# Kernel optimization log

Measured on AMD Instinct MI355X. Metric: run time of the kernel, lower is better.

## Reference

```python
import jax, jax.numpy as jnp
import numpy as np

B, T, D_IN, H, D2, D_OUT, N_CULT = 1024, 128, 32, 512, 256, 16, 32


def setup_inputs() -> dict:
    key = jax.random.key(0)
    ks = jax.random.split(key, 16)
    s = 0.05
    return {
        "input": jax.random.normal(ks[0], (B, T, D_IN), jnp.float32),
        "hn": jnp.zeros((1, B, H), jnp.float32),
        "cultivars": jax.random.randint(ks[1], (B, 1), 0, N_CULT, jnp.int32),
        "W1": jax.random.normal(ks[2], (D2, D_IN), jnp.float32) * s,
        "b1": jnp.zeros((D2,), jnp.float32),
        "W2": jax.random.normal(ks[3], (H, D2), jnp.float32) * s,
        "b2": jnp.zeros((H,), jnp.float32),
        "W_ih": jax.random.normal(ks[4], (3 * H, H), jnp.float32) * s,
        "W_hh": jax.random.normal(ks[5], (3 * H, H), jnp.float32) * s,
        "b_ih": jnp.zeros((3 * H,), jnp.float32),
        "b_hh": jnp.zeros((3 * H,), jnp.float32),
        "W3": jax.random.normal(ks[6], (D2, H), jnp.float32) * s,
        "b3": jnp.zeros((D2,), jnp.float32),
        "Wh": jax.random.normal(ks[7], (N_CULT, D_OUT, D2), jnp.float32) * s,
        "bh": jnp.zeros((N_CULT, D_OUT), jnp.float32),
    }


def _gru(x, h0, W_ih, W_hh, b_ih, b_hh):
    # x: [B,T,H]; h0: [B,H]. PyTorch GRU gate order: r, z, n.
    gx = jnp.einsum('bth,gh->btg', x, W_ih) + b_ih  # [B,T,3H]
    gx = jnp.swapaxes(gx, 0, 1)  # [T,B,3H]

    def step(h, gx_t):
        gh = h @ W_hh.T + b_hh
        xr, xz, xn = jnp.split(gx_t, 3, axis=-1)
        hr, hz, hnn = jnp.split(gh, 3, axis=-1)
        r = jax.nn.sigmoid(xr + hr)
        z = jax.nn.sigmoid(xz + hz)
        n = jnp.tanh(xn + r * hnn)
        h_new = (1.0 - z) * n + z * h
        return h_new, None

    h_last, _ = jax.lax.scan(step, h0, gx)
    return h_last  # [B,H]


def reference(input, hn, cultivars, W1, b1, W2, b2, W_ih, W_hh, b_ih, b_hh, W3, b3, Wh, bh):
    x = input @ W1.T + b1          # [B,T,D2]
    x = x @ W2.T + b2              # [B,T,H]
    h_last = _gru(x, hn[0], W_ih, W_hh, b_ih, b_hh)  # [B,H]
    hn_out = h_last[None]          # [1,B,H]
    out = jax.nn.relu(hn_out)
    out = jax.nn.relu(out @ W3.T + b3)[0]  # [B,D2]
    cult = cultivars[:, 0]
    # grouped per-sample head: params[i] = Wh[cult[i]] @ out[i] + bh[cult[i]]
    params = jnp.einsum('bd,bod->bo', out, Wh[cult]) + bh[cult]  # [B,D_OUT]
    return (params, hn_out)
```

## Files before the change

### kernel.cpp

```cpp
#include <hip/hip_runtime.h>


#define T_STEPS 128
#define PITCH   516
#define SLAB_ROWS 32

typedef __attribute__((ext_vector_type(8))) short short8;
typedef __attribute__((ext_vector_type(4))) float f32x4;
typedef __attribute__((ext_vector_type(4))) float float4v;
typedef unsigned short u16;
typedef unsigned long long u64;

static __device__ __forceinline__ u16 f2bf(float f) {
    unsigned int u = __builtin_bit_cast(unsigned int, f);
    u += 0x7FFFu + ((u >> 16) & 1u);
    return (u16)(u >> 16);
}
static __device__ __forceinline__ f32x4 mfma16(short8 a, short8 b, f32x4 c) {
    return __builtin_amdgcn_mfma_f32_16x16x32_bf16(a, b, c, 0, 0, 0);
}
static __device__ __forceinline__ void st_h16(u16* p, short8 v) {
    struct W { u64 a, b; } w = __builtin_bit_cast(W, v);
    u64* q = (u64*)p;
    __hip_atomic_store(q + 0, w.a, __ATOMIC_RELAXED, __HIP_MEMORY_SCOPE_AGENT);
    __hip_atomic_store(q + 1, w.b, __ATOMIC_RELAXED, __HIP_MEMORY_SCOPE_AGENT);
}
static __device__ __forceinline__ u64 ld_sc1_u64(const u16* p) {
    return __hip_atomic_load((const u64*)p, __ATOMIC_RELAXED, __HIP_MEMORY_SCOPE_AGENT);
}
static __device__ __forceinline__ short8 lds8(const u16* p) {
    u64 lo = *(const u64*)p;
    u64 hi = *(const u64*)(p + 4);
    struct W { u64 a, b; } w{lo, hi};
    return __builtin_bit_cast(short8, w);
}

#define WS_HBUF0 0
#define WS_HBUF1 1048576
#define WS_W21   2097152
#define WS_B21   2162688
#define WS_WEFF  2164736
#define WS_BEFF  2263040
#define WS_FLAGS 2269184

__global__ void k_prep0(const float* __restrict__ W1, const float* __restrict__ b1,
                        const float* __restrict__ W2, const float* __restrict__ b2,
                        float* __restrict__ W21, float* __restrict__ b21,
                        unsigned* __restrict__ flags) {
    if (blockIdx.x == 0)
        __hip_atomic_store(&flags[threadIdx.x], 0u, __ATOMIC_RELAXED, __HIP_MEMORY_SCOPE_AGENT);
    int gid = blockIdx.x * 256 + threadIdx.x;
    int k = gid >> 5, d = gid & 31;
    float acc = 0.f;
    for (int j = 0; j < 256; ++j)
        acc += W2[k * 256 + j] * W1[j * 32 + d];
    W21[k * 32 + d] = acc;
    if (d == 0) {
        float bb = b2[k];
        for (int j = 0; j < 256; ++j) bb += W2[k * 256 + j] * b1[j];
        b21[k] = bb;
    }
}

__global__ void k_prep1(const float* __restrict__ W_ih, const float* __restrict__ b_ih,
                        const float* __restrict__ W21, const float* __restrict__ b21,
                        u16* __restrict__ Weff, float* __restrict__ beff) {
    int gid = blockIdx.x * 256 + threadIdx.x;
    int g = gid >> 5, d = gid & 31;
    float acc = 0.f;
    for (int k = 0; k < 512; ++k)
        acc += W_ih[g * 512 + k] * W21[k * 32 + d];
    Weff[g * 32 + d] = f2bf(acc);
    if (d == 0) {
        float bb = b_ih[g];
        for (int k = 0; k < 512; ++k) bb += W_ih[g * 512 + k] * b21[k];
        beff[g] = bb;
    }
}

static __device__ __forceinline__ void bar_arrive(unsigned* gflags, int slot, unsigned v) {
    __syncthreads();
    if (threadIdx.x == 0)
        __hip_atomic_store(&gflags[slot], v, __ATOMIC_RELAXED, __HIP_MEMORY_SCOPE_AGENT);
}
static __device__ __forceinline__ void bar_wait(const unsigned* gflags, unsigned v) {
    if (threadIdx.x < 64) {
        int idx = threadIdx.x & 7;
        for (;;) {
            unsigned f = __hip_atomic_load(&gflags[idx], __ATOMIC_RELAXED, __HIP_MEMORY_SCOPE_AGENT);
            if (__ballot(f >= v) == ~0ull) break;
            __builtin_amdgcn_s_sleep(1);
        }
    }
    __syncthreads();
}

__launch_bounds__(256, 1)
__global__ void k_gru(const float* __restrict__ input, const float* __restrict__ hn,
                      const float* __restrict__ W_hh, const float* __restrict__ b_hh,
                      const u16* __restrict__ Weff, const float* __restrict__ beff,
                      u16* __restrict__ hbuf0, u16* __restrict__ hbuf1,
                      unsigned* __restrict__ flags, float* __restrict__ hn_out) {
    __shared__ __align__(16) u16 slab[SLAB_ROWS * PITCH];

    const int tid  = threadIdx.x;
    const int wave = tid >> 6, lane = tid & 63;
    const int col_l = lane & 15, quad = lane >> 4;
    const int blk = blockIdx.x;
    const int grp = blk & 31, colg = blk >> 5;
    const int grpbase = grp * 32;
    const int cb = colg * 64 + wave * 16;
    unsigned* gflags = flags + grp * 8;

    {
        int b = grpbase + colg * 4 + wave;
        const float* src = hn + (size_t)b * 512 + lane * 8;
        short8 v;
        #pragma unroll
        for (int e = 0; e < 8; ++e) v[e] = (short)f2bf(src[e]);
        st_h16(hbuf0 + (size_t)b * 512 + lane * 8, v);
    }
    short8 whhf[3][16];
    #pragma unroll
    for (int g3 = 0; g3 < 3; ++g3) {
        const float* wrow = W_hh + (size_t)(g3 * 512 + cb + col_l) * 512;
        #pragma unroll
        for (int kc = 0; kc < 16; ++kc) {
            const float* p = wrow + kc * 32 + quad * 8;
            short8 v;
            #pragma unroll
            for (int e = 0; e < 8; ++e) v[e] = (short)f2bf(p[e]);
            whhf[g3][kc] = v;
        }
    }
    short8 bwx[3];
    float bx[3], bhh[3];
    #pragma unroll
    for (int g3 = 0; g3 < 3; ++g3) {
        int nr = g3 * 512 + cb + col_l;
        bwx[g3] = *(const short8*)(Weff + nr * 32 + quad * 8);
        bx[g3]  = beff[nr];
        bhh[g3] = b_hh[nr];
    }
    float hs[2][4];
    #pragma unroll
    for (int m = 0; m < 2; ++m)
        #pragma unroll
        for (int i = 0; i < 4; ++i)
            hs[m][i] = hn[(size_t)(grpbase + m * 16 + quad * 4 + i) * 512 + cb + col_l];

    bar_arrive(gflags, colg, 1u);

    u16* bufs[2] = { hbuf0, hbuf1 };
    #pragma unroll 1
    for (int t = 0; t < T_STEPS; ++t) {
        const u16* hsrc = bufs[t & 1];
        u16* hdst = bufs[(t + 1) & 1];

        float xf[2][8];
        #pragma unroll
        for (int m = 0; m < 2; ++m) {
            const float* xp = input + (size_t)(grpbase + m * 16 + col_l) * 4096 + t * 32 + quad * 8;
            float4v a = *(const float4v*)xp;
            float4v b = *(const float4v*)(xp + 4);
            #pragma unroll
            for (int e = 0; e < 4; ++e) { xf[m][e] = a[e]; xf[m][4 + e] = b[e]; }
        }

        bar_wait(gflags, (unsigned)(t + 1));

        {
            u64 stg[16];
            #pragma unroll
            for (int r8 = 0; r8 < 8; ++r8) {
                int r = (wave * 8 + r8 + colg * 4) & 31;
                #pragma unroll
                for (int j = 0; j < 2; ++j)
                    stg[r8 * 2 + j] = ld_sc1_u64(hsrc + (size_t)(grpbase + r) * 512 + j * 256 + lane * 4);
            }
            #pragma unroll
            for (int r8 = 0; r8 < 8; ++r8) {
                int r = (wave * 8 + r8 + colg * 4) & 31;
                #pragma unroll
                for (int j = 0; j < 2; ++j)
                    *(u64*)&slab[r * PITCH + j * 256 + lane * 4] = stg[r8 * 2 + j];
            }
        }
        __syncthreads();

        #pragma unroll
        for (int m = 0; m < 2; ++m) {
            short8 ax;
            #pragma unroll
            for (int e = 0; e < 8; ++e) ax[e] = (short)f2bf(xf[m][e]);
            f32x4 z4 = { 0.f, 0.f, 0.f, 0.f };
            f32x4 ar  = mfma16(ax, bwx[0], z4);
            f32x4 az  = mfma16(ax, bwx[1], z4);
            f32x4 anx = mfma16(ax, bwx[2], z4);
            f32x4 anh = z4;
            const int arow = (m * 16 + col_l) * PITCH;
            #pragma unroll
            for (int kc = 0; kc < 16; ++kc) {
                short8 a = lds8(slab + arow + kc * 32 + quad * 8);
                ar  = mfma16(a, whhf[0][kc], ar);
                az  = mfma16(a, whhf[1][kc], az);
                anh = mfma16(a, whhf[2][kc], anh);
            }
            #pragma unroll
            for (int i = 0; i < 4; ++i) {
                float r = 1.f / (1.f + __expf(-(ar[i] + bx[0] + bhh[0])));
                float z = 1.f / (1.f + __expf(-(az[i] + bx[1] + bhh[1])));
                float np = anx[i] + bx[2] + r * (anh[i] + bhh[2]);
                float e  = __expf(-2.f * fabsf(np));
                float nn = __builtin_copysignf((1.f - e) / (1.f + e), np);
                float h  = (1.f - z) * nn + z * hs[m][i];
                hs[m][i] = h;
                int b = grpbase + m * 16 + quad * 4 + i;
                __hip_atomic_store(&hdst[(size_t)b * 512 + cb + col_l], f2bf(h),
                                   __ATOMIC_RELAXED, __HIP_MEMORY_SCOPE_AGENT);
            }
        }
        if (t < T_STEPS - 1)
            bar_arrive(gflags, colg, (unsigned)(t + 2));
    }
    #pragma unroll
    for (int m = 0; m < 2; ++m)
        #pragma unroll
        for (int i = 0; i < 4; ++i)
            hn_out[(size_t)(grpbase + m * 16 + quad * 4 + i) * 512 + cb + col_l] = hs[m][i];
}

__launch_bounds__(256)
__global__ void k_head(const u16* __restrict__ hfin, const float* __restrict__ W3,
                       const float* __restrict__ b3, const int* __restrict__ cult,
                       const float* __restrict__ Wh, const float* __restrict__ bh,
                       float* __restrict__ params) {
    __shared__ float out2[16][264];
    const int tid = threadIdx.x, wave = tid >> 6, lane = tid & 63;
    const int col_l = lane & 15, quad = lane >> 4;
    const int bbase = blockIdx.x * 16;

    f32x4 z4 = { 0.f, 0.f, 0.f, 0.f };
    f32x4 acc[4];
    #pragma unroll
    for (int nt = 0; nt < 4; ++nt) acc[nt] = z4;

    #pragma unroll
    for (int kc = 0; kc < 16; ++kc) {
        short8 a = *(const short8*)(hfin + (size_t)(bbase + col_l) * 512 + kc * 32 + quad * 8);
        #pragma unroll
        for (int e = 0; e < 8; ++e) {
            u16 v = (u16)a[e];
            a[e] = (short)((v & 0x8000u) ? 0 : v);
        }
        #pragma unroll
        for (int nt = 0; nt < 4; ++nt) {
            int nrow = wave * 64 + nt * 16 + col_l;
            const float* wr = W3 + (size_t)nrow * 512 + kc * 32 + quad * 8;
            short8 b;
            #pragma unroll
            for (int e = 0; e < 8; ++e) b[e] = (short)f2bf(wr[e]);
            acc[nt] = mfma16(a, b, acc[nt]);
        }
    }
    #pragma unroll
    for (int nt = 0; nt < 4; ++nt) {
        int ncol = wave * 64 + nt * 16 + col_l;
        float bias = b3[ncol];
        #pragma unroll
        for (int i = 0; i < 4; ++i) {
            float v = acc[nt][i] + bias;
            out2[quad * 4 + i][ncol] = v > 0.f ? v : 0.f;
        }
    }
    __syncthreads();
    int b_local = tid >> 4, o2 = tid & 15;
    int batch = bbase + b_local;
    int c = cult[batch];
    float acc2 = bh[c * 16 + o2];
    const float* wrow = Wh + (size_t)(c * 16 + o2) * 256;
    for (int d = 0; d < 256; ++d) acc2 += out2[b_local][d] * wrow[d];
    params[(size_t)batch * 16 + o2] = acc2;
}

extern "C" void kernel_launch(void* const* d_in, const int* in_sizes, int n_in,
                              void* d_out, int out_size, void* d_ws, size_t ws_size,
                              hipStream_t stream) {
    (void)in_sizes; (void)n_in; (void)out_size; (void)ws_size;
    const float* input = (const float*)d_in[0];
    const float* hn    = (const float*)d_in[1];
    const int*   cult  = (const int*)d_in[2];
    const float* W1    = (const float*)d_in[3];
    const float* b1    = (const float*)d_in[4];
    const float* W2    = (const float*)d_in[5];
    const float* b2    = (const float*)d_in[6];
    const float* W_ih  = (const float*)d_in[7];
    const float* W_hh  = (const float*)d_in[8];
    const float* b_ih  = (const float*)d_in[9];
    const float* b_hh  = (const float*)d_in[10];
    const float* W3    = (const float*)d_in[11];
    const float* b3    = (const float*)d_in[12];
    const float* Wh    = (const float*)d_in[13];
    const float* bh    = (const float*)d_in[14];

    char* ws = (char*)d_ws;
    u16*      hbuf0 = (u16*)(ws + WS_HBUF0);
    u16*      hbuf1 = (u16*)(ws + WS_HBUF1);
    float*    W21   = (float*)(ws + WS_W21);
    float*    b21   = (float*)(ws + WS_B21);
    u16*      Weff  = (u16*)(ws + WS_WEFF);
    float*    beff  = (float*)(ws + WS_BEFF);
    unsigned* flags = (unsigned*)(ws + WS_FLAGS);

    float* out    = (float*)d_out;
    float* params = out;
    float* hnout  = out + 16384;

    k_prep0<<<64, 256, 0, stream>>>(W1, b1, W2, b2, W21, b21, flags);
    k_prep1<<<192, 256, 0, stream>>>(W_ih, b_ih, W21, b21, Weff, beff);
    k_gru<<<256, 256, 0, stream>>>(input, hn, W_hh, b_hh, Weff, beff,
                                   hbuf0, hbuf1, flags, hnout);
    k_head<<<64, 256, 0, stream>>>(hbuf0, W3, b3, cult, Wh, bh, params);
}
```

Baseline: 741.8 us.

## Split GRU batch groups into 16-row groups across 512 blocks

Doubles the number of persistent GRU blocks from 256 to 512 by halving the batch rows each block handles (16 instead of 32), with 64 groups of 8 column blocks. Launch bounds are raised to allow two blocks per CU, and the input-projection MFMAs are hoisted before the barrier wait so they overlap the spin. Each block now reloads its W_hh slice into registers while doing half the recurrent work per step, which shortens the serial per-step path. The costs are more barrier flags, doubled total W_hh register loading, and co-residency requirements for the spin barrier under the higher register pressure of two blocks per CU.

```diff
diff --git a/kernel.cpp b/kernel.cpp
--- a/kernel.cpp
+++ b/kernel.cpp
@@ -3,7 +3,7 @@
 
 #define T_STEPS 128
 #define PITCH   516
-#define SLAB_ROWS 32
+#define SLAB_ROWS 16
 
 typedef __attribute__((ext_vector_type(8))) short short8;
 typedef __attribute__((ext_vector_type(4))) float f32x4;
@@ -47,8 +47,10 @@
                         const float* __restrict__ W2, const float* __restrict__ b2,
                         float* __restrict__ W21, float* __restrict__ b21,
                         unsigned* __restrict__ flags) {
-    if (blockIdx.x == 0)
+    if (blockIdx.x == 0) {
         __hip_atomic_store(&flags[threadIdx.x], 0u, __ATOMIC_RELAXED, __HIP_MEMORY_SCOPE_AGENT);
+        __hip_atomic_store(&flags[256 + threadIdx.x], 0u, __ATOMIC_RELAXED, __HIP_MEMORY_SCOPE_AGENT);
+    }
     int gid = blockIdx.x * 256 + threadIdx.x;
     int k = gid >> 5, d = gid & 31;
     float acc = 0.f;
@@ -95,7 +97,7 @@
     __syncthreads();
 }
 
-__launch_bounds__(256, 1)
+__launch_bounds__(256, 2)
 __global__ void k_gru(const float* __restrict__ input, const float* __restrict__ hn,
                       const float* __restrict__ W_hh, const float* __restrict__ b_hh,
                       const u16* __restrict__ Weff, const float* __restrict__ beff,
@@ -107,18 +109,22 @@
     const int wave = tid >> 6, lane = tid & 63;
     const int col_l = lane & 15, quad = lane >> 4;
     const int blk = blockIdx.x;
-    const int grp = blk & 31, colg = blk >> 5;
-    const int grpbase = grp * 32;
+    const int grp = (blk & 31) | ((blk >> 8) << 5);
+    const int colg = (blk >> 5) & 7;
+    const int grpbase = grp * 16;
     const int cb = colg * 64 + wave * 16;
     unsigned* gflags = flags + grp * 8;
 
-    {
-        int b = grpbase + colg * 4 + wave;
-        const float* src = hn + (size_t)b * 512 + lane * 8;
-        short8 v;
-        #pragma unroll
-        for (int e = 0; e < 8; ++e) v[e] = (short)f2bf(src[e]);
-        st_h16(hbuf0 + (size_t)b * 512 + lane * 8, v);
+    if (colg == 0) {
+        #pragma unroll
+        for (int r4 = 0; r4 < 4; ++r4) {
+            int b = grpbase + wave * 4 + r4;
+            const float* src = hn + (size_t)b * 512 + lane * 8;
+            short8 v;
+            #pragma unroll
+            for (int e = 0; e < 8; ++e) v[e] = (short)f2bf(src[e]);
+            st_h16(hbuf0 + (size_t)b * 512 + lane * 8, v);
+        }
     }
     short8 whhf[3][16];
     #pragma unroll
@@ -142,12 +148,10 @@
         bx[g3]  = beff[nr];
         bhh[g3] = b_hh[nr];
     }
-    float hs[2][4];
-    #pragma unroll
-    for (int m = 0; m < 2; ++m)
-        #pragma unroll
-        for (int i = 0; i < 4; ++i)
-            hs[m][i] = hn[(size_t)(grpbase + m * 16 + quad * 4 + i) * 512 + cb + col_l];
+    float hs[4];
+    #pragma unroll
+    for (int i = 0; i < 4; ++i)
+        hs[i] = hn[(size_t)(grpbase + quad * 4 + i) * 512 + cb + col_l];
 
     bar_arrive(gflags, colg, 1u);
 
@@ -157,77 +161,68 @@
         const u16* hsrc = bufs[t & 1];
         u16* hdst = bufs[(t + 1) & 1];
 
-        float xf[2][8];
-        #pragma unroll
-        for (int m = 0; m < 2; ++m) {
-            const float* xp = input + (size_t)(grpbase + m * 16 + col_l) * 4096 + t * 32 + quad * 8;
+        short8 ax;
+        {
+            const float* xp = input + (size_t)(grpbase + col_l) * 4096 + t * 32 + quad * 8;
             float4v a = *(const float4v*)xp;
             float4v b = *(const float4v*)(xp + 4);
             #pragma unroll
-            for (int e = 0; e < 4; ++e) { xf[m][e] = a[e]; xf[m][4 + e] = b[e]; }
-        }
+            for (int e = 0; e < 4; ++e) { ax[e] = (short)f2bf(a[e]); ax[4 + e] = (short)f2bf(b[e]); }
+        }
+        f32x4 z4 = { 0.f, 0.f, 0.f, 0.f };
+        f32x4 ar  = mfma16(ax, bwx[0], z4);
+        f32x4 az  = mfma16(ax, bwx[1], z4);
+        f32x4 anx = mfma16(ax, bwx[2], z4);
+        f32x4 anh = z4;
 
         bar_wait(gflags, (unsigned)(t + 1));
 
         {
-            u64 stg[16];
-            #pragma unroll
-            for (int r8 = 0; r8 < 8; ++r8) {
-                int r = (wave * 8 + r8 + colg * 4) & 31;
+            u64 stg[8];
+            #pragma unroll
+            for (int r4 = 0; r4 < 4; ++r4) {
+                int r = (wave * 4 + r4 + colg * 2) & 15;
                 #pragma unroll
                 for (int j = 0; j < 2; ++j)
-                    stg[r8 * 2 + j] = ld_sc1_u64(hsrc + (size_t)(grpbase + r) * 512 + j * 256 + lane * 4);
+                    stg[r4 * 2 + j] = ld_sc1_u64(hsrc + (size_t)(grpbase + r) * 512 + j * 256 + lane * 4);
             }
             #pragma unroll
-            for (int r8 = 0; r8 < 8; ++r8) {
-                int r = (wave * 8 + r8 + colg * 4) & 31;
+            for (int r4 = 0; r4 < 4; ++r4) {
+                int r = (wave * 4 + r4 + colg * 2) & 15;
                 #pragma unroll
                 for (int j = 0; j < 2; ++j)
-                    *(u64*)&slab[r * PITCH + j * 256 + lane * 4] = stg[r8 * 2 + j];
+                    *(u64*)&slab[r * PITCH + j * 256 + lane * 4] = stg[r4 * 2 + j];
             }
         }
         __syncthreads();
 
-        #pragma unroll
-        for (int m = 0; m < 2; ++m) {
-            short8 ax;
-            #pragma unroll
-            for (int e = 0; e < 8; ++e) ax[e] = (short)f2bf(xf[m][e]);
-            f32x4 z4 = { 0.f, 0.f, 0.f, 0.f };
-            f32x4 ar  = mfma16(ax, bwx[0], z4);
-            f32x4 az  = mfma16(ax, bwx[1], z4);
-            f32x4 anx = mfma16(ax, bwx[2], z4);
-            f32x4 anh = z4;
-            const int arow = (m * 16 + col_l) * PITCH;
-            #pragma unroll
-            for (int kc = 0; kc < 16; ++kc) {
-                short8 a = lds8(slab + arow + kc * 32 + quad * 8);
-                ar  = mfma16(a, whhf[0][kc], ar);
-                az  = mfma16(a, whhf[1][kc], az);
-                anh = mfma16(a, whhf[2][kc], anh);
-            }
-            #pragma unroll
-            for (int i = 0; i < 4; ++i) {
-                float r = 1.f / (1.f + __expf(-(ar[i] + bx[0] + bhh[0])));
-                float z = 1.f / (1.f + __expf(-(az[i] + bx[1] + bhh[1])));
-                float np = anx[i] + bx[2] + r * (anh[i] + bhh[2]);
-                float e  = __expf(-2.f * fabsf(np));
-                float nn = __builtin_copysignf((1.f - e) / (1.f + e), np);
-                float h  = (1.f - z) * nn + z * hs[m][i];
-                hs[m][i] = h;
-                int b = grpbase + m * 16 + quad * 4 + i;
-                __hip_atomic_store(&hdst[(size_t)b * 512 + cb + col_l], f2bf(h),
-                                   __ATOMIC_RELAXED, __HIP_MEMORY_SCOPE_AGENT);
-            }
+        const int arow = col_l * PITCH;
+        #pragma unroll
+        for (int kc = 0; kc < 16; ++kc) {
+            short8 a = lds8(slab + arow + kc * 32 + quad * 8);
+            ar  = mfma16(a, whhf[0][kc], ar);
+            az  = mfma16(a, whhf[1][kc], az);
+            anh = mfma16(a, whhf[2][kc], anh);
+        }
+        #pragma unroll
+        for (int i = 0; i < 4; ++i) {
+            float r = 1.f / (1.f + __expf(-(ar[i] + bx[0] + bhh[0])));
+            float z = 1.f / (1.f + __expf(-(az[i] + bx[1] + bhh[1])));
+            float np = anx[i] + bx[2] + r * (anh[i] + bhh[2]);
+            float e  = __expf(-2.f * fabsf(np));
+            float nn = __builtin_copysignf((1.f - e) / (1.f + e), np);
+            float h  = (1.f - z) * nn + z * hs[i];
+            hs[i] = h;
+            int b = grpbase + quad * 4 + i;
+            __hip_atomic_store(&hdst[(size_t)b * 512 + cb + col_l], f2bf(h),
+                               __ATOMIC_RELAXED, __HIP_MEMORY_SCOPE_AGENT);
         }
         if (t < T_STEPS - 1)
             bar_arrive(gflags, colg, (unsigned)(t + 2));
     }
     #pragma unroll
-    for (int m = 0; m < 2; ++m)
-        #pragma unroll
-        for (int i = 0; i < 4; ++i)
-            hn_out[(size_t)(grpbase + m * 16 + quad * 4 + i) * 512 + cb + col_l] = hs[m][i];
+    for (int i = 0; i < 4; ++i)
+        hn_out[(size_t)(grpbase + quad * 4 + i) * 512 + cb + col_l] = hs[i];
 }
 
 __launch_bounds__(256)
@@ -318,7 +313,7 @@
 
     k_prep0<<<64, 256, 0, stream>>>(W1, b1, W2, b2, W21, b21, flags);
     k_prep1<<<192, 256, 0, stream>>>(W_ih, b_ih, W21, b21, Weff, beff);
-    k_gru<<<256, 256, 0, stream>>>(input, hn, W_hh, b_hh, Weff, beff,
+    k_gru<<<512, 256, 0, stream>>>(input, hn, W_hh, b_hh, Weff, beff,
                                    hbuf0, hbuf1, flags, hnout);
     k_head<<<64, 256, 0, stream>>>(hbuf0, W3, b3, cult, Wh, bh, params);
 }
```

Result: slower. 779.9 us (+5.1%).

## Add runtime-probed fast per-step barrier using workgroup-scope atomics and direct LDS DMA

Applied to the files above, without the earlier changes.

At startup each group of 8 blocks checks whether plain (non-coherent) global writes from its partner blocks become visible, using a token write and read-back through global-to-LDS DMA. If the check passes, the per-step sync switches to workgroup-scope atomics and plain stores, and the hidden-state slab is pulled straight into LDS with global_load_lds instead of going through registers. The input-projection MFMAs are also issued before the barrier wait so they overlap it, and the LDS pitch changes for 16-byte reads. The risk is correctness: it bets that the 8 blocks of a group share a cache. The visibility probe may pass by chance while later steps read stale data.

```diff
diff --git a/kernel.cpp b/kernel.cpp
--- a/kernel.cpp
+++ b/kernel.cpp
@@ -2,7 +2,7 @@
 
 
 #define T_STEPS 128
-#define PITCH   516
+#define PITCH   520
 #define SLAB_ROWS 32
 
 typedef __attribute__((ext_vector_type(8))) short short8;
@@ -11,6 +11,13 @@
 typedef unsigned short u16;
 typedef unsigned long long u64;
 
+#define DMA16(g, l) __builtin_amdgcn_global_load_lds( \
+    (const __attribute__((address_space(1))) void*)(g), \
+    (__attribute__((address_space(3))) void*)(l), 16, 0, 1)
+#define DMA4(g, l) __builtin_amdgcn_global_load_lds( \
+    (const __attribute__((address_space(1))) void*)(g), \
+    (__attribute__((address_space(3))) void*)(l), 4, 0, 1)
+
 static __device__ __forceinline__ u16 f2bf(float f) {
     unsigned int u = __builtin_bit_cast(unsigned int, f);
     u += 0x7FFFu + ((u >> 16) & 1u);
@@ -27,12 +34,6 @@
 }
 static __device__ __forceinline__ u64 ld_sc1_u64(const u16* p) {
     return __hip_atomic_load((const u64*)p, __ATOMIC_RELAXED, __HIP_MEMORY_SCOPE_AGENT);
-}
-static __device__ __forceinline__ short8 lds8(const u16* p) {
-    u64 lo = *(const u64*)p;
-    u64 hi = *(const u64*)(p + 4);
-    struct W { u64 a, b; } w{lo, hi};
-    return __builtin_bit_cast(short8, w);
 }
 
 #define WS_HBUF0 0
@@ -41,14 +42,21 @@
 #define WS_B21   2162688
 #define WS_WEFF  2164736
 #define WS_BEFF  2263040
-#define WS_FLAGS 2269184
+#define WS_SFLAG 2269184
+#define WS_FFLAG 2270208
+#define WS_TEST  2274304
+#define WS_OK    2282496
+#define WS_TOKS  2283520
 
 __global__ void k_prep0(const float* __restrict__ W1, const float* __restrict__ b1,
                         const float* __restrict__ W2, const float* __restrict__ b2,
                         float* __restrict__ W21, float* __restrict__ b21,
-                        unsigned* __restrict__ flags) {
-    if (blockIdx.x == 0)
-        __hip_atomic_store(&flags[threadIdx.x], 0u, __ATOMIC_RELAXED, __HIP_MEMORY_SCOPE_AGENT);
+                        unsigned* __restrict__ sflags, unsigned* __restrict__ fflags) {
+    if (blockIdx.x == 0) {
+        int t = threadIdx.x;
+        __hip_atomic_store(&sflags[t], 0u, __ATOMIC_RELAXED, __HIP_MEMORY_SCOPE_AGENT);
+        __hip_atomic_store(&fflags[(t >> 3) * 32 + (t & 7)], 0u, __ATOMIC_RELAXED, __HIP_MEMORY_SCOPE_AGENT);
+    }
     int gid = blockIdx.x * 256 + threadIdx.x;
     int k = gid >> 5, d = gid & 31;
     float acc = 0.f;
@@ -78,12 +86,12 @@
     }
 }
 
-static __device__ __forceinline__ void bar_arrive(unsigned* gflags, int slot, unsigned v) {
+static __device__ __forceinline__ void bar_arrive_slow(unsigned* gflags, int slot, unsigned v) {
     __syncthreads();
     if (threadIdx.x == 0)
         __hip_atomic_store(&gflags[slot], v, __ATOMIC_RELAXED, __HIP_MEMORY_SCOPE_AGENT);
 }
-static __device__ __forceinline__ void bar_wait(const unsigned* gflags, unsigned v) {
+static __device__ __forceinline__ void bar_wait_slow(const unsigned* gflags, unsigned v) {
     if (threadIdx.x < 64) {
         int idx = threadIdx.x & 7;
         for (;;) {
@@ -94,14 +102,30 @@
     }
     __syncthreads();
 }
+static __device__ __forceinline__ void bar_wait_fast(unsigned* gff, unsigned v) {
+    if (threadIdx.x < 64) {
+        for (;;) {
+            unsigned f = v;
+            if (threadIdx.x < 8)
+                f = __hip_atomic_fetch_add(&gff[threadIdx.x], 0u,
+                                           __ATOMIC_RELAXED, __HIP_MEMORY_SCOPE_WORKGROUP);
+            if (__ballot(f >= v) == ~0ull) break;
+            __builtin_amdgcn_s_sleep(1);
+        }
+    }
+    __syncthreads();
+}
 
 __launch_bounds__(256, 1)
 __global__ void k_gru(const float* __restrict__ input, const float* __restrict__ hn,
                       const float* __restrict__ W_hh, const float* __restrict__ b_hh,
                       const u16* __restrict__ Weff, const float* __restrict__ beff,
                       u16* __restrict__ hbuf0, u16* __restrict__ hbuf1,
-                      unsigned* __restrict__ flags, float* __restrict__ hn_out) {
+                      unsigned* __restrict__ sflags, unsigned* __restrict__ fflags,
+                      unsigned* __restrict__ testc, unsigned* __restrict__ okbuf,
+                      unsigned* __restrict__ tokslot, float* __restrict__ hn_out) {
     __shared__ __align__(16) u16 slab[SLAB_ROWS * PITCH];
+    __shared__ unsigned fast_sh;
 
     const int tid  = threadIdx.x;
     const int wave = tid >> 6, lane = tid & 63;
@@ -110,7 +134,9 @@
     const int grp = blk & 31, colg = blk >> 5;
     const int grpbase = grp * 32;
     const int cb = colg * 64 + wave * 16;
-    unsigned* gflags = flags + grp * 8;
+    unsigned* gflags = sflags + grp * 8;
+    unsigned* gff    = fflags + grp * 32;
+    unsigned* trow   = testc + grp * 64;
 
     {
         int b = grpbase + colg * 4 + wave;
@@ -120,6 +146,16 @@
         for (int e = 0; e < 8; ++e) v[e] = (short)f2bf(src[e]);
         st_h16(hbuf0 + (size_t)b * 512 + lane * 8, v);
     }
+    unsigned tok = 0;
+    if (colg == 0) {
+        u64 rt = __builtin_amdgcn_s_memrealtime();
+        tok = ((unsigned)rt ^ (unsigned)(rt >> 32)) | 1u;
+        if (tid < 64) trow[tid] = tok;
+        if (tid == 0)
+            __hip_atomic_store(&tokslot[grp], tok, __ATOMIC_RELAXED, __HIP_MEMORY_SCOPE_AGENT);
+    }
+    bar_arrive_slow(gflags, colg, 1u);
+
     short8 whhf[3][16];
     #pragma unroll
     for (int g3 = 0; g3 < 3; ++g3) {
@@ -149,7 +185,34 @@
         for (int i = 0; i < 4; ++i)
             hs[m][i] = hn[(size_t)(grpbase + m * 16 + quad * 4 + i) * 512 + cb + col_l];
 
-    bar_arrive(gflags, colg, 1u);
+    bar_wait_slow(gflags, 1u);
+    unsigned tokv = __hip_atomic_load(&tokslot[grp], __ATOMIC_RELAXED, __HIP_MEMORY_SCOPE_AGENT);
+    unsigned* hsk = (unsigned*)slab;
+    if (tid < 64) DMA4(trow + lane, hsk + lane);
+    bar_arrive_slow(gflags, colg, 2u);
+    bar_wait_slow(gflags, 2u);
+    if (colg == 0 && tid < 64) trow[tid] = tokv + 1u;
+    bar_arrive_slow(gflags, colg, 3u);
+    bar_wait_slow(gflags, 3u);
+    if (tid < 64) DMA4(trow + lane, hsk + 64 + lane);
+    __syncthreads();
+    if (tid < 64) {
+        unsigned ok = (hsk[64 + lane] == tokv + 1u) ? 1u : 0u;
+        unsigned allok = (__ballot(ok != 0u) == ~0ull) ? 1u : 0u;
+        if (tid == 0)
+            __hip_atomic_store(&okbuf[grp * 8 + colg], allok,
+                               __ATOMIC_RELAXED, __HIP_MEMORY_SCOPE_AGENT);
+    }
+    bar_arrive_slow(gflags, colg, 4u);
+    bar_wait_slow(gflags, 4u);
+    if (tid == 0) {
+        unsigned all = 1u;
+        for (int c = 0; c < 8; ++c)
+            all &= __hip_atomic_load(&okbuf[grp * 8 + c], __ATOMIC_RELAXED, __HIP_MEMORY_SCOPE_AGENT);
+        fast_sh = all;
+    }
+    __syncthreads();
+    const bool fast = (fast_sh != 0u);
 
     u16* bufs[2] = { hbuf0, hbuf1 };
     #pragma unroll 1
@@ -157,19 +220,35 @@
         const u16* hsrc = bufs[t & 1];
         u16* hdst = bufs[(t + 1) & 1];
 
-        float xf[2][8];
+        short8 ax[2];
         #pragma unroll
         for (int m = 0; m < 2; ++m) {
             const float* xp = input + (size_t)(grpbase + m * 16 + col_l) * 4096 + t * 32 + quad * 8;
             float4v a = *(const float4v*)xp;
             float4v b = *(const float4v*)(xp + 4);
             #pragma unroll
-            for (int e = 0; e < 4; ++e) { xf[m][e] = a[e]; xf[m][4 + e] = b[e]; }
-        }
-
-        bar_wait(gflags, (unsigned)(t + 1));
-
-        {
+            for (int e = 0; e < 4; ++e) { ax[m][e] = (short)f2bf(a[e]); ax[m][4 + e] = (short)f2bf(b[e]); }
+        }
+        f32x4 z4 = { 0.f, 0.f, 0.f, 0.f };
+        f32x4 ar[2], az[2], anx[2], anh[2];
+        #pragma unroll
+        for (int m = 0; m < 2; ++m) {
+            ar[m]  = mfma16(ax[m], bwx[0], z4);
+            az[m]  = mfma16(ax[m], bwx[1], z4);
+            anx[m] = mfma16(ax[m], bwx[2], z4);
+            anh[m] = z4;
+        }
+
+        if (fast) {
+            if (t > 0) bar_wait_fast(gff, (unsigned)t);
+            #pragma unroll
+            for (int r8 = 0; r8 < 8; ++r8) {
+                int r = (wave * 8 + r8 + colg * 4) & 31;
+                DMA16(hsrc + (size_t)(grpbase + r) * 512 + lane * 8,
+                      slab + r * PITCH + lane * 8);
+            }
+        } else {
+            if (t > 0) bar_wait_slow(gflags, (unsigned)(t + 4));
             u64 stg[16];
             #pragma unroll
             for (int r8 = 0; r8 < 8; ++r8) {
@@ -190,38 +269,42 @@
 
         #pragma unroll
         for (int m = 0; m < 2; ++m) {
-            short8 ax;
-            #pragma unroll
-            for (int e = 0; e < 8; ++e) ax[e] = (short)f2bf(xf[m][e]);
-            f32x4 z4 = { 0.f, 0.f, 0.f, 0.f };
-            f32x4 ar  = mfma16(ax, bwx[0], z4);
-            f32x4 az  = mfma16(ax, bwx[1], z4);
-            f32x4 anx = mfma16(ax, bwx[2], z4);
-            f32x4 anh = z4;
             const int arow = (m * 16 + col_l) * PITCH;
             #pragma unroll
             for (int kc = 0; kc < 16; ++kc) {
-                short8 a = lds8(slab + arow + kc * 32 + quad * 8);
-                ar  = mfma16(a, whhf[0][kc], ar);
-                az  = mfma16(a, whhf[1][kc], az);
-                anh = mfma16(a, whhf[2][kc], anh);
+                short8 a = *(const short8*)(slab + arow + kc * 32 + quad * 8);
+                ar[m]  = mfma16(a, whhf[0][kc], ar[m]);
+                az[m]  = mfma16(a, whhf[1][kc], az[m]);
+                anh[m] = mfma16(a, whhf[2][kc], anh[m]);
             }
             #pragma unroll
             for (int i = 0; i < 4; ++i) {
-                float r = 1.f / (1.f + __expf(-(ar[i] + bx[0] + bhh[0])));
-                float z = 1.f / (1.f + __expf(-(az[i] + bx[1] + bhh[1])));
-                float np = anx[i] + bx[2] + r * (anh[i] + bhh[2]);
+                float r = 1.f / (1.f + __expf(-(ar[m][i] + bx[0] + bhh[0])));
+                float z = 1.f / (1.f + __expf(-(az[m][i] + bx[1] + bhh[1])));
+                float np = anx[m][i] + bx[2] + r * (anh[m][i] + bhh[2]);
                 float e  = __expf(-2.f * fabsf(np));
                 float nn = __builtin_copysignf((1.f - e) / (1.f + e), np);
                 float h  = (1.f - z) * nn + z * hs[m][i];
                 hs[m][i] = h;
                 int b = grpbase + m * 16 + quad * 4 + i;
-                __hip_atomic_store(&hdst[(size_t)b * 512 + cb + col_l], f2bf(h),
-                                   __ATOMIC_RELAXED, __HIP_MEMORY_SCOPE_AGENT);
-            }
-        }
-        if (t < T_STEPS - 1)
-            bar_arrive(gflags, colg, (unsigned)(t + 2));
+                u16 hb = f2bf(h);
+                if (fast)
+                    hdst[(size_t)b * 512 + cb + col_l] = hb;
+                else
+                    __hip_atomic_store(&hdst[(size_t)b * 512 + cb + col_l], hb,
+                                       __ATOMIC_RELAXED, __HIP_MEMORY_SCOPE_AGENT);
+            }
+        }
+        if (t < T_STEPS - 1) {
+            if (fast) {
+                __syncthreads();
+                if (tid == 0)
+                    __hip_atomic_fetch_max(&gff[colg], (unsigned)(t + 1),
+                                           __ATOMIC_RELAXED, __HIP_MEMORY_SCOPE_WORKGROUP);
+            } else {
+                bar_arrive_slow(gflags, colg, (unsigned)(t + 5));
+            }
+        }
     }
     #pragma unroll
     for (int m = 0; m < 2; ++m)
@@ -304,21 +387,26 @@
     const float* bh    = (const float*)d_in[14];
 
     char* ws = (char*)d_ws;
-    u16*      hbuf0 = (u16*)(ws + WS_HBUF0);
-    u16*      hbuf1 = (u16*)(ws + WS_HBUF1);
-    float*    W21   = (float*)(ws + WS_W21);
-    float*    b21   = (float*)(ws + WS_B21);
-    u16*      Weff  = (u16*)(ws + WS_WEFF);
-    float*    beff  = (float*)(ws + WS_BEFF);
-    unsigned* flags = (unsigned*)(ws + WS_FLAGS);
+    u16*      hbuf0   = (u16*)(ws + WS_HBUF0);
+    u16*      hbuf1   = (u16*)(ws + WS_HBUF1);
+    float*    W21     = (float*)(ws + WS_W21);
+    float*    b21     = (float*)(ws + WS_B21);
+    u16*      Weff    = (u16*)(ws + WS_WEFF);
+    float*    beff    = (float*)(ws + WS_BEFF);
+    unsigned* sflags  = (unsigned*)(ws + WS_SFLAG);
+    unsigned* fflags  = (unsigned*)(ws + WS_FFLAG);
+    unsigned* testc   = (unsigned*)(ws + WS_TEST);
+    unsigned* okbuf   = (unsigned*)(ws + WS_OK);
+    unsigned* tokslot = (unsigned*)(ws + WS_TOKS);
 
     float* out    = (float*)d_out;
     float* params = out;
     float* hnout  = out + 16384;
 
-    k_prep0<<<64, 256, 0, stream>>>(W1, b1, W2, b2, W21, b21, flags);
+    k_prep0<<<64, 256, 0, stream>>>(W1, b1, W2, b2, W21, b21, sflags, fflags);
     k_prep1<<<192, 256, 0, stream>>>(W_ih, b_ih, W21, b21, Weff, beff);
     k_gru<<<256, 256, 0, stream>>>(input, hn, W_hh, b_hh, Weff, beff,
-                                   hbuf0, hbuf1, flags, hnout);
+                                   hbuf0, hbuf1, sflags, fflags, testc, okbuf,
+                                   tokslot, hnout);
     k_head<<<64, 256, 0, stream>>>(hbuf0, W3, b3, cult, Wh, bh, params);
 }
```

Measured after the change: 828.3 us. 1.12x slower.

## Use per-wave flags for the GRU grid barrier and hoist input projection

Applied to the files above, without the earlier changes.

Replaces the block-level arrive (syncthreads followed by one store per block) with per-wave flag publication, so each wave signals its own slot after draining its stores. Every wave now polls all 32 flags of its group without sleeping, rather than only the first wave polling and then syncing. The input-projection MFMAs are moved ahead of the barrier wait so they overlap the spin. This shortens the critical path of each of the 128 serial recurrent steps, at the cost of more polling traffic and higher register pressure.

```diff
diff --git a/kernel.cpp b/kernel.cpp
--- a/kernel.cpp
+++ b/kernel.cpp
@@ -47,8 +47,12 @@
                         const float* __restrict__ W2, const float* __restrict__ b2,
                         float* __restrict__ W21, float* __restrict__ b21,
                         unsigned* __restrict__ flags) {
-    if (blockIdx.x == 0)
-        __hip_atomic_store(&flags[threadIdx.x], 0u, __ATOMIC_RELAXED, __HIP_MEMORY_SCOPE_AGENT);
+    if (blockIdx.x == 0) {
+        int t = threadIdx.x;
+        #pragma unroll
+        for (int j = 0; j < 4; ++j)
+            __hip_atomic_store(&flags[j * 256 + t], 0u, __ATOMIC_RELAXED, __HIP_MEMORY_SCOPE_AGENT);
+    }
     int gid = blockIdx.x * 256 + threadIdx.x;
     int k = gid >> 5, d = gid & 31;
     float acc = 0.f;
@@ -78,21 +82,17 @@
     }
 }
 
-static __device__ __forceinline__ void bar_arrive(unsigned* gflags, int slot, unsigned v) {
-    __syncthreads();
-    if (threadIdx.x == 0)
+static __device__ __forceinline__ void wave_publish(unsigned* gflags, int slot, unsigned v) {
+    __builtin_amdgcn_s_waitcnt(0);
+    if ((threadIdx.x & 63) == 0)
         __hip_atomic_store(&gflags[slot], v, __ATOMIC_RELAXED, __HIP_MEMORY_SCOPE_AGENT);
 }
 static __device__ __forceinline__ void bar_wait(const unsigned* gflags, unsigned v) {
-    if (threadIdx.x < 64) {
-        int idx = threadIdx.x & 7;
-        for (;;) {
-            unsigned f = __hip_atomic_load(&gflags[idx], __ATOMIC_RELAXED, __HIP_MEMORY_SCOPE_AGENT);
-            if (__ballot(f >= v) == ~0ull) break;
-            __builtin_amdgcn_s_sleep(1);
-        }
-    }
-    __syncthreads();
+    int idx = threadIdx.x & 31;
+    for (;;) {
+        unsigned f = __hip_atomic_load(&gflags[idx], __ATOMIC_RELAXED, __HIP_MEMORY_SCOPE_AGENT);
+        if (__ballot(f >= v) == ~0ull) break;
+    }
 }
 
 __launch_bounds__(256, 1)
@@ -110,7 +110,8 @@
     const int grp = blk & 31, colg = blk >> 5;
     const int grpbase = grp * 32;
     const int cb = colg * 64 + wave * 16;
-    unsigned* gflags = flags + grp * 8;
+    const int slot = colg * 4 + wave;
+    unsigned* gflags = flags + grp * 32;
 
     {
         int b = grpbase + colg * 4 + wave;
@@ -120,6 +121,8 @@
         for (int e = 0; e < 8; ++e) v[e] = (short)f2bf(src[e]);
         st_h16(hbuf0 + (size_t)b * 512 + lane * 8, v);
     }
+    wave_publish(gflags, slot, 1u);
+
     short8 whhf[3][16];
     #pragma unroll
     for (int g3 = 0; g3 < 3; ++g3) {
@@ -149,22 +152,29 @@
         for (int i = 0; i < 4; ++i)
             hs[m][i] = hn[(size_t)(grpbase + m * 16 + quad * 4 + i) * 512 + cb + col_l];
 
-    bar_arrive(gflags, colg, 1u);
-
     u16* bufs[2] = { hbuf0, hbuf1 };
     #pragma unroll 1
     for (int t = 0; t < T_STEPS; ++t) {
         const u16* hsrc = bufs[t & 1];
         u16* hdst = bufs[(t + 1) & 1];
 
-        float xf[2][8];
+        short8 ax[2];
         #pragma unroll
         for (int m = 0; m < 2; ++m) {
             const float* xp = input + (size_t)(grpbase + m * 16 + col_l) * 4096 + t * 32 + quad * 8;
             float4v a = *(const float4v*)xp;
             float4v b = *(const float4v*)(xp + 4);
             #pragma unroll
-            for (int e = 0; e < 4; ++e) { xf[m][e] = a[e]; xf[m][4 + e] = b[e]; }
+            for (int e = 0; e < 4; ++e) { ax[m][e] = (short)f2bf(a[e]); ax[m][4 + e] = (short)f2bf(b[e]); }
+        }
+        f32x4 z4 = { 0.f, 0.f, 0.f, 0.f };
+        f32x4 ar[2], az[2], anx[2], anh[2];
+        #pragma unroll
+        for (int m = 0; m < 2; ++m) {
+            ar[m]  = mfma16(ax[m], bwx[0], z4);
+            az[m]  = mfma16(ax[m], bwx[1], z4);
+            anx[m] = mfma16(ax[m], bwx[2], z4);
+            anh[m] = z4;
         }
 
         bar_wait(gflags, (unsigned)(t + 1));
@@ -190,27 +200,19 @@
 
         #pragma unroll
         for (int m = 0; m < 2; ++m) {
-            short8 ax;
-            #pragma unroll
-            for (int e = 0; e < 8; ++e) ax[e] = (short)f2bf(xf[m][e]);
-            f32x4 z4 = { 0.f, 0.f, 0.f, 0.f };
-            f32x4 ar  = mfma16(ax, bwx[0], z4);
-            f32x4 az  = mfma16(ax, bwx[1], z4);
-            f32x4 anx = mfma16(ax, bwx[2], z4);
-            f32x4 anh = z4;
             const int arow = (m * 16 + col_l) * PITCH;
             #pragma unroll
             for (int kc = 0; kc < 16; ++kc) {
                 short8 a = lds8(slab + arow + kc * 32 + quad * 8);
-                ar  = mfma16(a, whhf[0][kc], ar);
-                az  = mfma16(a, whhf[1][kc], az);
-                anh = mfma16(a, whhf[2][kc], anh);
+                ar[m]  = mfma16(a, whhf[0][kc], ar[m]);
+                az[m]  = mfma16(a, whhf[1][kc], az[m]);
+                anh[m] = mfma16(a, whhf[2][kc], anh[m]);
             }
             #pragma unroll
             for (int i = 0; i < 4; ++i) {
-                float r = 1.f / (1.f + __expf(-(ar[i] + bx[0] + bhh[0])));
-                float z = 1.f / (1.f + __expf(-(az[i] + bx[1] + bhh[1])));
-                float np = anx[i] + bx[2] + r * (anh[i] + bhh[2]);
+                float r = 1.f / (1.f + __expf(-(ar[m][i] + bx[0] + bhh[0])));
+                float z = 1.f / (1.f + __expf(-(az[m][i] + bx[1] + bhh[1])));
+                float np = anx[m][i] + bx[2] + r * (anh[m][i] + bhh[2]);
                 float e  = __expf(-2.f * fabsf(np));
                 float nn = __builtin_copysignf((1.f - e) / (1.f + e), np);
                 float h  = (1.f - z) * nn + z * hs[m][i];
@@ -221,7 +223,8 @@
             }
         }
         if (t < T_STEPS - 1)
-            bar_arrive(gflags, colg, (unsigned)(t + 2));
+            wave_publish(gflags, slot, (unsigned)(t + 2));
+        __syncthreads();
     }
     #pragma unroll
     for (int m = 0; m < 2; ++m)
```

New measurement: 755.8 us. Within noise of the previous version (+1.9%).
